# Kernel tuning notes

Measured on AMD Instinct MI355X. Metric: run time of the kernel, lower is better.

## Reference

```python
import jax, jax.numpy as jnp
import numpy as np

N_LAYERS = 6
D_MODEL = 512
D_FFN = 2048
N_STATE = 64
KSIZE = 31
BATCH = 8
SEQ = 2048
IN_SIZE = 80


def _ln(x, g, b, eps=1e-5):
    m = jnp.mean(x, axis=-1, keepdims=True)
    v = jnp.mean((x - m) ** 2, axis=-1, keepdims=True)
    return (x - m) * jax.lax.rsqrt(v + eps) * g + b


def _ffn(x, g, b, w1, b1, w2, b2):
    # LayerNorm -> Linear(D->F) -> GELU -> Linear(F->D)  (PositionalwiseFeedForward)
    h = jax.nn.gelu(_ln(x, g, b) @ w1 + b1)
    return h @ w2 + b2


def _dss(x, lam_re, lam_im, c_re, c_im, d_skip, log_dt, w_out, b_out):
    # Diagonal state-space (DSS-EXP): generate length-T kernel from diagonal poles,
    # apply causal conv via FFT, skip D*u, GELU, GLU output projection.
    Bx, T, H = x.shape
    dt = jnp.exp(log_dt)
    lam = -jnp.exp(lam_re) + 1j * lam_im                        # [N] stable poles (Re<0)
    P = jnp.exp(lam[:, None] * (dt * jnp.arange(T))[None, :])   # [N, T]
    C = c_re + 1j * c_im                                        # [H, N]
    kern = jnp.einsum('hn,nt->ht', C, P).real * dt              # [H, T]
    u = x.transpose(0, 2, 1)                                    # [B, H, T]
    n = 2 * T
    y = jnp.fft.irfft(jnp.fft.rfft(u, n=n) * jnp.fft.rfft(kern, n=n), n=n)[..., :T]
    y = y + d_skip[None, :, None] * u
    y = jax.nn.gelu(y.transpose(0, 2, 1))                       # [B, T, H]
    z = y @ w_out + b_out                                       # [B, T, 2H]
    a, g = jnp.split(z, 2, axis=-1)
    return a * jax.nn.sigmoid(g)                                # GLU


def _conv_module(x, g1, b1, bw, bb, dw, db, g2, b2, lw, lb):
    # LN -> 1x1 conv to 2D + GLU -> depthwise conv (SAME, k=31) -> LN -> GELU -> Linear
    y = _ln(x, g1, b1)
    y = y @ bw.T + bb                                           # [B, T, 2D]
    a, g = jnp.split(y, 2, axis=-1)
    y = a * jax.nn.sigmoid(g)                                   # GLU over channels
    yc = y.transpose(0, 2, 1)                                   # [B, D, T]
    yc = jax.lax.conv_general_dilated(
        yc, dw[:, None, :], (1,), 'SAME',
        feature_group_count=yc.shape[1],
        dimension_numbers=('NCH', 'OIH', 'NCH'))
    yc = yc + db[None, :, None]
    y = jax.nn.gelu(_ln(yc.transpose(0, 2, 1), g2, b2))
    return y @ lw.T + lb


def _forward(src, speaker_embs, src_w, src_b,
             ffn1_ln_g, ffn1_ln_b, ffn1_w1, ffn1_b1, ffn1_w2, ffn1_b2,
             norm1_g, norm1_b,
             lam_re, lam_im, c_re, c_im, ssm_d, log_dt, dss_out_w, dss_out_b,
             conv_ln_g, conv_ln_b, bneck_w, bneck_b, dw_w, dw_b,
             conv_ln2_g, conv_ln2_b, conv_lin_w, conv_lin_b,
             ffn2_ln_g, ffn2_ln_b, ffn2_w1, ffn2_b1, ffn2_w2, ffn2_b2,
             norm2_g, norm2_b, final_g, final_b):
    x = src @ src_w + src_b                                     # custom_src_module Linear
    for i in range(N_LAYERS):
        x = x + 0.5 * _ffn(x, ffn1_ln_g[i], ffn1_ln_b[i], ffn1_w1[i], ffn1_b1[i], ffn1_w2[i], ffn1_b2[i])
        skip = x
        x = _ln(x, norm1_g[i], norm1_b[i])
        x = _dss(x, lam_re[i], lam_im[i], c_re[i], c_im[i], ssm_d[i], log_dt[i], dss_out_w[i], dss_out_b[i])
        x = x + skip
        x = x + _conv_module(x, conv_ln_g[i], conv_ln_b[i], bneck_w[i], bneck_b[i], dw_w[i], dw_b[i],
                             conv_ln2_g[i], conv_ln2_b[i], conv_lin_w[i], conv_lin_b[i])
        x = _ln(x + 0.5 * _ffn(x, ffn2_ln_g[i], ffn2_ln_b[i], ffn2_w1[i], ffn2_b1[i], ffn2_w2[i], ffn2_b2[i]),
                norm2_g[i], norm2_b[i])
    x = _ln(x, final_g, final_b, eps=1e-6)
    return x + speaker_embs


def setup_inputs() -> dict:
    key = jax.random.key(0)
    ks = iter(jax.random.split(key, 64))
    def rn(shape, s=0.02):
        return (jax.random.normal(next(ks), shape) * s).astype(jnp.float32)
    L, D, F, N, K = N_LAYERS, D_MODEL, D_FFN, N_STATE, KSIZE
    return dict(
        src=jax.random.normal(next(ks), (BATCH, SEQ, IN_SIZE), dtype=jnp.float32),
        speaker_embs=jax.random.normal(next(ks), (BATCH, 1, D), dtype=jnp.float32),
        src_w=rn((IN_SIZE, D)), src_b=jnp.zeros((D,), jnp.float32),
        ffn1_ln_g=jnp.ones((L, D), jnp.float32), ffn1_ln_b=jnp.zeros((L, D), jnp.float32),
        ffn1_w1=rn((L, D, F)), ffn1_b1=jnp.zeros((L, F), jnp.float32),
        ffn1_w2=rn((L, F, D)), ffn1_b2=jnp.zeros((L, D), jnp.float32),
        norm1_g=jnp.ones((L, D), jnp.float32), norm1_b=jnp.zeros((L, D), jnp.float32),
        lam_re=rn((L, N), 0.5), lam_im=rn((L, N), 3.0),
        c_re=rn((L, D, N), 0.1), c_im=rn((L, D, N), 0.1),
        ssm_d=rn((L, D), 1.0), log_dt=jnp.full((L,), float(np.log(0.01)), jnp.float32),
        dss_out_w=rn((L, D, 2 * D)), dss_out_b=jnp.zeros((L, 2 * D), jnp.float32),
        conv_ln_g=jnp.ones((L, D), jnp.float32), conv_ln_b=jnp.zeros((L, D), jnp.float32),
        bneck_w=rn((L, 2 * D, D)), bneck_b=jnp.zeros((L, 2 * D), jnp.float32),
        dw_w=rn((L, D, K), 0.1), dw_b=jnp.zeros((L, D), jnp.float32),
        conv_ln2_g=jnp.ones((L, D), jnp.float32), conv_ln2_b=jnp.zeros((L, D), jnp.float32),
        conv_lin_w=rn((L, D, D)), conv_lin_b=jnp.zeros((L, D), jnp.float32),
        ffn2_ln_g=jnp.ones((L, D), jnp.float32), ffn2_ln_b=jnp.zeros((L, D), jnp.float32),
        ffn2_w1=rn((L, D, F)), ffn2_b1=jnp.zeros((L, F), jnp.float32),
        ffn2_w2=rn((L, F, D)), ffn2_b2=jnp.zeros((L, D), jnp.float32),
        norm2_g=jnp.ones((L, D), jnp.float32), norm2_b=jnp.zeros((L, D), jnp.float32),
        final_g=jnp.ones((D,), jnp.float32), final_b=jnp.zeros((D,), jnp.float32),
    )


def reference(src, speaker_embs, src_w, src_b,
              ffn1_ln_g, ffn1_ln_b, ffn1_w1, ffn1_b1, ffn1_w2, ffn1_b2,
              norm1_g, norm1_b,
              lam_re, lam_im, c_re, c_im, ssm_d, log_dt, dss_out_w, dss_out_b,
              conv_ln_g, conv_ln_b, bneck_w, bneck_b, dw_w, dw_b,
              conv_ln2_g, conv_ln2_b, conv_lin_w, conv_lin_b,
              ffn2_ln_g, ffn2_ln_b, ffn2_w1, ffn2_b1, ffn2_w2, ffn2_b2,
              norm2_g, norm2_b, final_g, final_b):
    return _forward(src, speaker_embs, src_w, src_b,
                    ffn1_ln_g, ffn1_ln_b, ffn1_w1, ffn1_b1, ffn1_w2, ffn1_b2,
                    norm1_g, norm1_b,
                    lam_re, lam_im, c_re, c_im, ssm_d, log_dt, dss_out_w, dss_out_b,
                    conv_ln_g, conv_ln_b, bneck_w, bneck_b, dw_w, dw_b,
                    conv_ln2_g, conv_ln2_b, conv_lin_w, conv_lin_b,
                    ffn2_ln_g, ffn2_ln_b, ffn2_w1, ffn2_b1, ffn2_w2, ffn2_b2,
                    norm2_g, norm2_b, final_g, final_b)
```

## Files before the change

kernel.cpp:

```cpp
#include <hip/hip_runtime.h>
#include <hip/hip_bf16.h>
#include <stdint.h>


#define NL 6
#define TT 2048
#define BB 8
#define DD 512
#define FF 2048
#define ROWS (BB*TT)

typedef __attribute__((ext_vector_type(4))) float f32x4;
typedef __attribute__((ext_vector_type(8))) short s16x8;

#define DEVI __device__ __forceinline__

DEVI float bf2f(uint32_t u) { union { uint32_t i; float f; } v; v.i = u << 16; return v.f; }
DEVI uint16_t f2bf(float f) {
    union { float f; uint32_t i; } v; v.f = f;
    uint32_t x = v.i;
    return (uint16_t)((x + 0x7fffu + ((x >> 16) & 1u)) >> 16);
}
DEVI float gelu_f(float x) {
    float x2 = x * x;
    float z  = x * fmaf(x2, 0.07135481627f, 1.5957691216f);
    return x * __builtin_amdgcn_rcpf(1.0f + __expf(-z));
}
DEVI float sigm(float x) { return __builtin_amdgcn_rcpf(1.0f + __expf(-x)); }

DEVI void gload16(const uint16_t* g, uint16_t* l) {
    __builtin_amdgcn_global_load_lds((const __attribute__((address_space(1))) void*)g,
                                     (__attribute__((address_space(3))) void*)l, 16, 0, 0);
}

__global__ void k_wtrans(const float* __restrict__ src, uint16_t* __restrict__ dst,
                         int K, int N) {
    __shared__ float tile[32][33];
    int l = blockIdx.z;
    const float* s = src + (size_t)l * K * N;
    uint16_t*    d = dst + (size_t)l * N * K;
    int n0 = blockIdx.x * 32, k0 = blockIdx.y * 32;
    int tx = threadIdx.x, ty = threadIdx.y;
#pragma unroll
    for (int i = 0; i < 4; i++) {
        int k = k0 + ty + i * 8;
        tile[ty + i * 8][tx] = s[(size_t)k * N + n0 + tx];
    }
    __syncthreads();
#pragma unroll
    for (int i = 0; i < 4; i++) {
        int n = n0 + ty + i * 8;
        d[(size_t)n * K + k0 + tx] = f2bf(tile[tx][ty + i * 8]);
    }
}
__global__ void k_wcvt(const float* __restrict__ src, uint16_t* __restrict__ dst, int n) {
    int i = blockIdx.x * 256 + threadIdx.x;
    if (i < n) dst[i] = f2bf(src[i]);
}
__global__ void k_dwt(const float* __restrict__ dw, float* __restrict__ dwt) {
    int i = blockIdx.x * 256 + threadIdx.x;
    int tot = NL * DD * 31;
    if (i >= tot) return;
    int l = i / (DD * 31), r = i % (DD * 31), d = r / 31, k = r % 31;
    dwt[(size_t)l * 31 * DD + k * DD + d] = dw[i];
}
__global__ void k_srcpad(const float* __restrict__ src, uint16_t* __restrict__ dst) {
    int i = blockIdx.x * 256 + threadIdx.x;
    if (i >= ROWS * 128) return;
    int r = i >> 7, c = i & 127;
    dst[i] = (c < 80) ? f2bf(src[(size_t)r * 80 + c]) : (uint16_t)0;
}
__global__ void k_wsrcpad(const float* __restrict__ w, uint16_t* __restrict__ dst) {
    int i = blockIdx.x * 256 + threadIdx.x;
    if (i >= DD * 128) return;
    int n = i >> 7, k = i & 127;
    dst[i] = (k < 80) ? f2bf(w[(size_t)k * DD + n]) : (uint16_t)0;
}

template <int MODE>
__global__ void k_ln(const float* __restrict__ in, void* __restrict__ outp,
                     const float* __restrict__ gam, const float* __restrict__ bet,
                     const float* __restrict__ spk, float eps) {
    int row  = blockIdx.x * 4 + (threadIdx.x >> 6);
    int lane = threadIdx.x & 63;
    const float* x = in + (size_t)row * DD;
    float4 a0 = *(const float4*)&x[lane * 4];
    float4 a1 = *(const float4*)&x[256 + lane * 4];
    float v[8] = {a0.x, a0.y, a0.z, a0.w, a1.x, a1.y, a1.z, a1.w};
    float s = 0.f, q = 0.f;
#pragma unroll
    for (int i = 0; i < 8; i++) { s += v[i]; q += v[i] * v[i]; }
#pragma unroll
    for (int m = 1; m < 64; m <<= 1) { s += __shfl_xor(s, m); q += __shfl_xor(q, m); }
    float mean = s * (1.0f / 512.0f);
    float var  = fmaxf(q * (1.0f / 512.0f) - mean * mean, 0.0f);
    float inv  = rsqrtf(var + eps);
    float4 g0 = *(const float4*)&gam[lane * 4];
    float4 g1 = *(const float4*)&gam[256 + lane * 4];
    float4 b0 = *(const float4*)&bet[lane * 4];
    float4 b1 = *(const float4*)&bet[256 + lane * 4];
    float gv[8] = {g0.x, g0.y, g0.z, g0.w, g1.x, g1.y, g1.z, g1.w};
    float bv[8] = {b0.x, b0.y, b0.z, b0.w, b1.x, b1.y, b1.z, b1.w};
    float y[8];
#pragma unroll
    for (int i = 0; i < 8; i++) y[i] = (v[i] - mean) * inv * gv[i] + bv[i];
    uint16_t* o = (uint16_t*)outp + (size_t)row * DD;
    uint2 p0, p1;
    p0.x = (uint32_t)f2bf(y[0]) | ((uint32_t)f2bf(y[1]) << 16);
    p0.y = (uint32_t)f2bf(y[2]) | ((uint32_t)f2bf(y[3]) << 16);
    p1.x = (uint32_t)f2bf(y[4]) | ((uint32_t)f2bf(y[5]) << 16);
    p1.y = (uint32_t)f2bf(y[6]) | ((uint32_t)f2bf(y[7]) << 16);
    *(uint2*)&o[lane * 4]       = p0;
    *(uint2*)&o[256 + lane * 4] = p1;
}

template <int M2>
__global__ void k_ln2(const float* __restrict__ in, float* __restrict__ X,
                      void* __restrict__ out2,
                      const float* __restrict__ g1, const float* __restrict__ b1,
                      const float* __restrict__ g2, const float* __restrict__ b2,
                      const float* __restrict__ spk, float eps2) {
    int row  = blockIdx.x * 4 + (threadIdx.x >> 6);
    int lane = threadIdx.x & 63;
    const float* x = in + (size_t)row * DD;
    float4 a0 = *(const float4*)&x[lane * 4];
    float4 a1 = *(const float4*)&x[256 + lane * 4];
    float v[8] = {a0.x, a0.y, a0.z, a0.w, a1.x, a1.y, a1.z, a1.w};
    float s = 0.f, q = 0.f;
#pragma unroll
    for (int i = 0; i < 8; i++) { s += v[i]; q += v[i] * v[i]; }
#pragma unroll
    for (int m = 1; m < 64; m <<= 1) { s += __shfl_xor(s, m); q += __shfl_xor(q, m); }
    float mean = s * (1.0f / 512.0f);
    float var  = fmaxf(q * (1.0f / 512.0f) - mean * mean, 0.0f);
    float inv  = rsqrtf(var + 1e-5f);
    float4 g0 = *(const float4*)&g1[lane * 4];
    float4 g1v = *(const float4*)&g1[256 + lane * 4];
    float4 b0 = *(const float4*)&b1[lane * 4];
    float4 b1v = *(const float4*)&b1[256 + lane * 4];
    float gv[8] = {g0.x, g0.y, g0.z, g0.w, g1v.x, g1v.y, g1v.z, g1v.w};
    float bv[8] = {b0.x, b0.y, b0.z, b0.w, b1v.x, b1v.y, b1v.z, b1v.w};
    float y[8];
    float s2 = 0.f, q2 = 0.f;
#pragma unroll
    for (int i = 0; i < 8; i++) {
        y[i] = (v[i] - mean) * inv * gv[i] + bv[i];
        s2 += y[i]; q2 += y[i] * y[i];
    }
    if (M2 == 6) {
        float* xo = X + (size_t)row * DD;
        *(float4*)&xo[lane * 4]       = make_float4(y[0], y[1], y[2], y[3]);
        *(float4*)&xo[256 + lane * 4] = make_float4(y[4], y[5], y[6], y[7]);
    }
#pragma unroll
    for (int m = 1; m < 64; m <<= 1) { s2 += __shfl_xor(s2, m); q2 += __shfl_xor(q2, m); }
    float mean2 = s2 * (1.0f / 512.0f);
    float var2  = fmaxf(q2 * (1.0f / 512.0f) - mean2 * mean2, 0.0f);
    float inv2  = rsqrtf(var2 + eps2);
    float4 G0 = *(const float4*)&g2[lane * 4];
    float4 G1 = *(const float4*)&g2[256 + lane * 4];
    float4 B0 = *(const float4*)&b2[lane * 4];
    float4 B1v = *(const float4*)&b2[256 + lane * 4];
    float Gv[8] = {G0.x, G0.y, G0.z, G0.w, G1.x, G1.y, G1.z, G1.w};
    float Bv[8] = {B0.x, B0.y, B0.z, B0.w, B1v.x, B1v.y, B1v.z, B1v.w};
    float z[8];
#pragma unroll
    for (int i = 0; i < 8; i++) z[i] = (y[i] - mean2) * inv2 * Gv[i] + Bv[i];
    if (M2 == 6) {
        uint16_t* o = (uint16_t*)out2 + (size_t)row * DD;
        uint2 p0, p1;
        p0.x = (uint32_t)f2bf(z[0]) | ((uint32_t)f2bf(z[1]) << 16);
        p0.y = (uint32_t)f2bf(z[2]) | ((uint32_t)f2bf(z[3]) << 16);
        p1.x = (uint32_t)f2bf(z[4]) | ((uint32_t)f2bf(z[5]) << 16);
        p1.y = (uint32_t)f2bf(z[6]) | ((uint32_t)f2bf(z[7]) << 16);
        *(uint2*)&o[lane * 4]       = p0;
        *(uint2*)&o[256 + lane * 4] = p1;
    } else {
        const float* sp = spk + (size_t)(row >> 11) * DD;
        float4 s0 = *(const float4*)&sp[lane * 4];
        float4 s1 = *(const float4*)&sp[256 + lane * 4];
        float* o = (float*)out2 + (size_t)row * DD;
        *(float4*)&o[lane * 4]       = make_float4(z[0]+s0.x, z[1]+s0.y, z[2]+s0.z, z[3]+s0.w);
        *(float4*)&o[256 + lane * 4] = make_float4(z[4]+s1.x, z[5]+s1.y, z[6]+s1.z, z[7]+s1.w);
    }
}

__global__ void k_gluln(const uint16_t* __restrict__ H, float* __restrict__ X,
                        uint16_t* __restrict__ out,
                        const float* __restrict__ gam, const float* __restrict__ bet) {
    int row  = blockIdx.x * 4 + (threadIdx.x >> 6);
    int lane = threadIdx.x & 63;
    const uint16_t* hr = H + (size_t)row * 1024;
    uint2 ha0 = *(const uint2*)&hr[lane * 4];
    uint2 ha1 = *(const uint2*)&hr[256 + lane * 4];
    uint2 hg0 = *(const uint2*)&hr[512 + lane * 4];
    uint2 hg1 = *(const uint2*)&hr[768 + lane * 4];
    uint32_t aw[4] = {ha0.x, ha0.y, ha1.x, ha1.y};
    uint32_t gw[4] = {hg0.x, hg0.y, hg1.x, hg1.y};
    float* xr = X + (size_t)row * DD;
    float4 x0 = *(const float4*)&xr[lane * 4];
    float4 x1 = *(const float4*)&xr[256 + lane * 4];
    float xv[8] = {x0.x, x0.y, x0.z, x0.w, x1.x, x1.y, x1.z, x1.w};
    float v[8];
#pragma unroll
    for (int p = 0; p < 4; p++) {
        float a0 = bf2f(aw[p] & 0xffffu), a1 = bf2f(aw[p] >> 16);
        float g0 = bf2f(gw[p] & 0xffffu), g1 = bf2f(gw[p] >> 16);
        v[2*p]   = xv[2*p]   + a0 * sigm(g0);
        v[2*p+1] = xv[2*p+1] + a1 * sigm(g1);
    }
    *(float4*)&xr[lane * 4]       = make_float4(v[0], v[1], v[2], v[3]);
    *(float4*)&xr[256 + lane * 4] = make_float4(v[4], v[5], v[6], v[7]);
    float s = 0.f, q = 0.f;
#pragma unroll
    for (int i = 0; i < 8; i++) { s += v[i]; q += v[i] * v[i]; }
#pragma unroll
    for (int m = 1; m < 64; m <<= 1) { s += __shfl_xor(s, m); q += __shfl_xor(q, m); }
    float mean = s * (1.0f / 512.0f);
    float var  = fmaxf(q * (1.0f / 512.0f) - mean * mean, 0.0f);
    float inv  = rsqrtf(var + 1e-5f);
    float4 g0 = *(const float4*)&gam[lane * 4];
    float4 g1 = *(const float4*)&gam[256 + lane * 4];
    float4 b0 = *(const float4*)&bet[lane * 4];
    float4 b1 = *(const float4*)&bet[256 + lane * 4];
    float gv[8] = {g0.x, g0.y, g0.z, g0.w, g1.x, g1.y, g1.z, g1.w};
    float bv[8] = {b0.x, b0.y, b0.z, b0.w, b1.x, b1.y, b1.z, b1.w};
    uint16_t* o = out + (size_t)row * DD;
    uint2 p0, p1;
    float y0 = (v[0]-mean)*inv*gv[0]+bv[0], y1 = (v[1]-mean)*inv*gv[1]+bv[1];
    float y2 = (v[2]-mean)*inv*gv[2]+bv[2], y3 = (v[3]-mean)*inv*gv[3]+bv[3];
    float y4 = (v[4]-mean)*inv*gv[4]+bv[4], y5 = (v[5]-mean)*inv*gv[5]+bv[5];
    float y6 = (v[6]-mean)*inv*gv[6]+bv[6], y7 = (v[7]-mean)*inv*gv[7]+bv[7];
    p0.x = (uint32_t)f2bf(y0) | ((uint32_t)f2bf(y1) << 16);
    p0.y = (uint32_t)f2bf(y2) | ((uint32_t)f2bf(y3) << 16);
    p1.x = (uint32_t)f2bf(y4) | ((uint32_t)f2bf(y5) << 16);
    p1.y = (uint32_t)f2bf(y6) | ((uint32_t)f2bf(y7) << 16);
    *(uint2*)&o[lane * 4]       = p0;
    *(uint2*)&o[256 + lane * 4] = p1;
}

template <int MODE, int BN>
__global__ __launch_bounds__(512, 2) void k_gemm3(
    const uint16_t* __restrict__ A, const uint16_t* __restrict__ Bt,
    const float* __restrict__ bias, int M, int N, int K,
    void* __restrict__ outp, float* __restrict__ X) {
    constexpr int MR = 8;
    constexpr int NR = BN / 64;
    constexpr int ABLK = 16;
    constexpr int BBLK = BN / 16;
    constexpr int APW = 2;
    constexpr int BPW = BBLK / 8;
    constexpr int LV  = APW + BPW;
    __shared__ __align__(16) uint16_t As[3][ABLK * 512];
    __shared__ __align__(16) uint16_t Bs[3][BBLK * 512];
    int tid = threadIdx.x;
    int wave = tid >> 6, lane = tid & 63;
    int l15 = lane & 15, l16 = lane >> 4;
    int wr = wave >> 2, wc = wave & 3;

    int nwg = gridDim.x;
    int q8  = nwg >> 3;
    int wg  = (blockIdx.x & 7) * q8 + (blockIdx.x >> 3);
    int nbx = M >> 8;
    int bx = wg % nbx, by = wg / nbx;
    int m0 = bx * 256, n0 = by * BN;

    const uint16_t* srcA[APW];
    const uint16_t* srcB[BPW];
#pragma unroll
    for (int p = 0; p < APW; p++) {
        int bi = wave * APW + p;
        srcA[p] = A + (size_t)(m0 + bi * 16 + l15) * K + l16 * 8;
    }
#pragma unroll
    for (int p = 0; p < BPW; p++) {
        int bi = wave * BPW + p;
        srcB[p] = Bt + (size_t)(n0 + bi * 16 + l15) * K + l16 * 8;
    }

    f32x4 acc[MR][NR];
#pragma unroll
    for (int i = 0; i < MR; i++)
#pragma unroll
        for (int j = 0; j < NR; j++) acc[i][j] = (f32x4){0.f, 0.f, 0.f, 0.f};

    auto STAGE = [&](int tt) {
        int b = tt % 3;
        int kof = tt << 5;
#pragma unroll
        for (int p = 0; p < APW; p++)
            gload16(srcA[p] + kof, &As[b][(wave * APW + p) * 512]);
#pragma unroll
        for (int p = 0; p < BPW; p++)
            gload16(srcB[p] + kof, &Bs[b][(wave * BPW + p) * 512]);
    };

    int nk = K >> 5;
    STAGE(0);
    STAGE(1);
    for (int t = 0; t < nk; ++t) {
        if (t + 1 < nk) {
            if (LV == 4) asm volatile("s_waitcnt vmcnt(4)" ::: "memory");
            else         asm volatile("s_waitcnt vmcnt(3)" ::: "memory");
        } else {
            asm volatile("s_waitcnt vmcnt(0)" ::: "memory");
        }
        __builtin_amdgcn_s_barrier();
        asm volatile("" ::: "memory");
        if (t + 2 < nk) STAGE(t + 2);
        int buf = t % 3;
        s16x8 af[MR], bfr[NR];
#pragma unroll
        for (int i = 0; i < MR; i++)
            af[i] = *(const s16x8*)&As[buf][(wr * MR + i) * 512 + lane * 8];
#pragma unroll
        for (int j = 0; j < NR; j++)
            bfr[j] = *(const s16x8*)&Bs[buf][(wc * NR + j) * 512 + lane * 8];
#pragma unroll
        for (int i = 0; i < MR; i++)
#pragma unroll
            for (int j = 0; j < NR; j++)
                acc[i][j] = __builtin_amdgcn_mfma_f32_16x16x32_bf16(af[i], bfr[j], acc[i][j], 0, 0, 0);
    }
#pragma unroll
    for (int i = 0; i < MR; i++) {
#pragma unroll
        for (int j = 0; j < NR; j++) {
            int gcol = n0 + wc * NR * 16 + j * 16 + l15;
            float bv = bias[gcol];
#pragma unroll
            for (int q = 0; q < 4; q++) {
                int grow = m0 + wr * MR * 16 + i * 16 + l16 * 4 + q;
                float v = acc[i][j][q] + bv;
                if (MODE == 0) {
                    ((uint16_t*)outp)[(size_t)grow * N + gcol] = f2bf(gelu_f(v));
                } else if (MODE == 1) {
                    ((uint16_t*)outp)[(size_t)grow * N + gcol] = f2bf(v);
                } else if (MODE == 2) {
                    X[(size_t)grow * DD + gcol] += 0.5f * v;
                } else if (MODE == 3) {
                    X[(size_t)grow * DD + gcol] += v;
                } else if (MODE == 4) {
                    ((float*)outp)[(size_t)grow * DD + gcol] =
                        X[(size_t)grow * DD + gcol] + 0.5f * v;
                } else {
                    X[(size_t)grow * DD + gcol] = v;
                }
            }
        }
    }
}

__global__ void k_tpose(const uint16_t* __restrict__ in, uint16_t* __restrict__ out,
                        int R, int C) {
    __shared__ uint16_t tile[32][33];
    size_t boff = (size_t)blockIdx.z * R * C;
    int c0 = blockIdx.x * 32, r0 = blockIdx.y * 32;
    int tx = threadIdx.x, ty = threadIdx.y;
#pragma unroll
    for (int i = 0; i < 4; i++)
        tile[ty + i * 8][tx] = in[boff + (size_t)(r0 + ty + i * 8) * C + c0 + tx];
    __syncthreads();
#pragma unroll
    for (int i = 0; i < 4; i++)
        out[boff + (size_t)(c0 + ty + i * 8) * R + r0 + tx] = tile[tx][ty + i * 8];
}

__global__ __launch_bounds__(64) void k_phiprep(
        const float* __restrict__ lam_re, const float* __restrict__ lam_im,
        const float* __restrict__ log_dt, uint16_t* __restrict__ PHI,
        float* __restrict__ A64f) {
    int l = blockIdx.x, n = threadIdx.x;
    float dt = expf(log_dt[l]);
    float lr = lam_re[l * 64 + n], li = lam_im[l * 64 + n];
    float mag = expf(-expf(lr) * dt), th = li * dt;
    float Are = mag * __cosf(th), Aim = mag * __sinf(th);
    float Pre = 1.f, Pim = 0.f;
    uint16_t* ph = PHI + (size_t)l * 8192;
    for (int tau = 0; tau < 64; tau++) {
        int s = 63 - tau;
        ph[n * 64 + s]        = f2bf(Pre);
        ph[(64 + n) * 64 + s] = f2bf(Pim);
        float nr = Pre * Are - Pim * Aim;
        float ni = Pre * Aim + Pim * Are;
        Pre = nr; Pim = ni;
    }
    A64f[l * 128 + 2 * n]     = Pre;
    A64f[l * 128 + 2 * n + 1] = Pim;
}

__global__ __launch_bounds__(64) void k_gprep(
        const float* __restrict__ lam_re, const float* __restrict__ lam_im,
        const float* __restrict__ c_re, const float* __restrict__ c_im,
        const float* __restrict__ ssm_d, const float* __restrict__ log_dt,
        int l, uint16_t* __restrict__ G) {
    int h = blockIdx.x, n = threadIdx.x;
    __shared__ float klds[64];
    float dt = expf(log_dt[l]);
    float lr = lam_re[l * 64 + n], li = lam_im[l * 64 + n];
    float mag = expf(-expf(lr) * dt), th = li * dt;
    float Are = mag * __cosf(th), Aim = mag * __sinf(th);
    float Cre = c_re[(size_t)l * DD * 64 + h * 64 + n];
    float Cim = c_im[(size_t)l * DD * 64 + h * 64 + n];
    uint16_t* Gh = G + (size_t)h * 64 * 192;
    float Pre = 1.f, Pim = 0.f;
    for (int r = 0; r < 64; r++) {
        float t = Cre * Pre - Cim * Pim;
        float s = t;
        s += __shfl_xor(s, 1);  s += __shfl_xor(s, 2);  s += __shfl_xor(s, 4);
        s += __shfl_xor(s, 8);  s += __shfl_xor(s, 16); s += __shfl_xor(s, 32);
        if (n == 0) klds[r] = dt * s;
        float nr = Pre * Are - Pim * Aim;
        float ni = Pre * Aim + Pim * Are;
        float wre = dt * (Cre * nr - Cim * ni);
        float wim = dt * (Cre * ni + Cim * nr);
        Gh[r * 192 + 64 + n]  = f2bf(wre);
        Gh[r * 192 + 128 + n] = f2bf(-wim);
        Pre = nr; Pim = ni;
    }
    __syncthreads();
    float dh = ssm_d[l * DD + h];
    for (int r = 0; r < 64; r++) {
        int c = n;
        float val = (c < r) ? klds[r - c] : (c == r ? klds[0] + dh : 0.f);
        Gh[r * 192 + c] = f2bf(val);
    }
}

__global__ __launch_bounds__(256) void k_pass1(
        const uint16_t* __restrict__ u, const uint16_t* __restrict__ PHI,
        uint16_t* __restrict__ E) {
    __shared__ __align__(16) uint16_t Phs[128 * 72];
    int tid = threadIdx.x;
    for (int v = tid; v < 1024; v += 256) {
        int row = v >> 3, kb = v & 7;
        *(s16x8*)&Phs[row * 72 + kb * 8] = *(const s16x8*)&PHI[row * 64 + kb * 8];
    }
    __syncthreads();
    int wave = tid >> 6, lane = tid & 63;
    int l15 = lane & 15, l16 = lane >> 4;
    int m0 = (wave & 1) * 64;
    int colbase = blockIdx.x * 128 + (wave >> 1) * 64;
    f32x4 acc[4][4];
#pragma unroll
    for (int i = 0; i < 4; i++)
#pragma unroll
        for (int j = 0; j < 4; j++) acc[i][j] = (f32x4){0.f, 0.f, 0.f, 0.f};
#pragma unroll
    for (int kt = 0; kt < 64; kt += 32) {
        s16x8 a[4], b[4];
#pragma unroll
        for (int i = 0; i < 4; i++)
            a[i] = *(const s16x8*)&Phs[(m0 + i * 16 + l15) * 72 + kt + l16 * 8];
#pragma unroll
        for (int j = 0; j < 4; j++)
            b[j] = *(const s16x8*)(u + (size_t)(colbase + j * 16 + l15) * 64 + kt + l16 * 8);
#pragma unroll
        for (int i = 0; i < 4; i++)
#pragma unroll
            for (int j = 0; j < 4; j++)
                acc[i][j] = __builtin_amdgcn_mfma_f32_16x16x32_bf16(a[i], b[j], acc[i][j], 0, 0, 0);
    }
#pragma unroll
    for (int i = 0; i < 4; i++)
#pragma unroll
        for (int j = 0; j < 4; j++) {
            int col = colbase + j * 16 + l15;
            int r0  = m0 + i * 16 + l16 * 4;
            uint32_t p0 = (uint32_t)f2bf(acc[i][j][0]) | ((uint32_t)f2bf(acc[i][j][1]) << 16);
            uint32_t p1 = (uint32_t)f2bf(acc[i][j][2]) | ((uint32_t)f2bf(acc[i][j][3]) << 16);
            *(uint2*)&E[(size_t)col * 128 + r0] = make_uint2(p0, p1);
        }
}

__global__ void k_pass2(const uint16_t* __restrict__ E, const float* __restrict__ A64f,
                        int l, uint16_t* __restrict__ Sp) {
    int gid = blockIdx.x * 256 + threadIdx.x;
    int n = gid & 63, bh = gid >> 6;
    int b = bh >> 9, h = bh & 511;
    float2 A = *(const float2*)&A64f[l * 128 + 2 * n];
    float Sre = 0.f, Sim = 0.f;
    const uint16_t* Eb = E + (size_t)bh * 32 * 128;
    uint16_t* So = Sp + (size_t)h * 32768 + (size_t)b * 32 * 128;
    for (int i = 0; i < 32; i++) {
        So[i * 128 + n]      = f2bf(Sre);
        So[i * 128 + 64 + n] = f2bf(Sim);
        float er = bf2f((uint32_t)Eb[i * 128 + n]);
        float ei = bf2f((uint32_t)Eb[i * 128 + 64 + n]);
        float nr = A.x * Sre - A.y * Sim + er;
        float ni = A.x * Sim + A.y * Sre + ei;
        Sre = nr; Sim = ni;
    }
}

__global__ __launch_bounds__(256) void k_pass3(
        const uint16_t* __restrict__ G, const uint16_t* __restrict__ u,
        const uint16_t* __restrict__ Sp, uint16_t* __restrict__ Y) {
    __shared__ __align__(16) uint16_t Gs[64 * 200];
    int h = blockIdx.x, tid = threadIdx.x;
    for (int v = tid; v < 1536; v += 256) {
        int row = v / 24, kb = v % 24;
        *(s16x8*)&Gs[row * 200 + kb * 8] = *(const s16x8*)&G[(size_t)h * 12288 + row * 192 + kb * 8];
    }
    __syncthreads();
    int wave = tid >> 6, lane = tid & 63;
    int l15 = lane & 15, l16 = lane >> 4;
    int wn = wave * 64;
    const uint16_t* uh = u + (size_t)h * TT;
    const uint16_t* sh = Sp + (size_t)h * 32768;
    f32x4 acc[4][4];
#pragma unroll
    for (int i = 0; i < 4; i++)
#pragma unroll
        for (int j = 0; j < 4; j++) acc[i][j] = (f32x4){0.f, 0.f, 0.f, 0.f};
#pragma unroll
    for (int kt = 0; kt < 192; kt += 32) {
        s16x8 a[4], b[4];
#pragma unroll
        for (int i = 0; i < 4; i++)
            a[i] = *(const s16x8*)&Gs[(i * 16 + l15) * 200 + kt + l16 * 8];
#pragma unroll
        for (int j = 0; j < 4; j++) {
            int col = wn + j * 16 + l15;
            const uint16_t* src;
            if (kt < 64)
                src = uh + (size_t)(col >> 5) * (DD * TT) + (col & 31) * 64 + kt + l16 * 8;
            else
                src = sh + (size_t)col * 128 + (kt - 64) + l16 * 8;
            b[j] = *(const s16x8*)src;
        }
#pragma unroll
        for (int i = 0; i < 4; i++)
#pragma unroll
            for (int j = 0; j < 4; j++)
                acc[i][j] = __builtin_amdgcn_mfma_f32_16x16x32_bf16(a[i], b[j], acc[i][j], 0, 0, 0);
    }
#pragma unroll
    for (int i = 0; i < 4; i++)
#pragma unroll
        for (int j = 0; j < 4; j++) {
            int col = wn + j * 16 + l15;
            int r0  = i * 16 + l16 * 4;
            uint16_t* dst = Y + (size_t)(col >> 5) * (DD * TT) + (size_t)h * TT + (col & 31) * 64 + r0;
            uint32_t p0 = (uint32_t)f2bf(acc[i][j][0]) | ((uint32_t)f2bf(acc[i][j][1]) << 16);
            uint32_t p1 = (uint32_t)f2bf(acc[i][j][2]) | ((uint32_t)f2bf(acc[i][j][3]) << 16);
            *(uint2*)&dst[0] = make_uint2(p0, p1);
        }
}

__global__ void k_tgelu(const uint16_t* __restrict__ y, uint16_t* __restrict__ out) {
    __shared__ uint16_t tile[32][33];
    int b = blockIdx.z;
    int t0 = blockIdx.x * 32, h0 = blockIdx.y * 32;
    int tx = threadIdx.x, ty = threadIdx.y;
    const uint16_t* yb = y + (size_t)b * DD * TT;
#pragma unroll
    for (int i = 0; i < 4; i++) {
        int h = h0 + ty + i * 8;
        tile[ty + i * 8][tx] = f2bf(gelu_f(bf2f((uint32_t)yb[(size_t)h * TT + t0 + tx])));
    }
    __syncthreads();
    uint16_t* ob = out + (size_t)b * TT * DD;
#pragma unroll
    for (int i = 0; i < 4; i++) {
        int t = t0 + ty + i * 8;
        ob[(size_t)t * DD + h0 + tx] = tile[tx][ty + i * 8];
    }
}

__global__ void k_glu(const uint16_t* __restrict__ z, uint16_t* __restrict__ out) {
    int i = blockIdx.x * 256 + threadIdx.x;
    int r = i >> 8;
    int c = (i & 255) * 2;
    uint32_t av = *(const uint32_t*)&z[(size_t)r * 1024 + c];
    uint32_t gv = *(const uint32_t*)&z[(size_t)r * 1024 + 512 + c];
    float a0 = bf2f(av & 0xffffu), a1 = bf2f(av >> 16);
    float g0 = bf2f(gv & 0xffffu), g1 = bf2f(gv >> 16);
    float v0 = a0 * sigm(g0), v1 = a1 * sigm(g1);
    uint32_t p = (uint32_t)f2bf(v0) | ((uint32_t)f2bf(v1) << 16);
    *(uint32_t*)&out[(size_t)r * DD + c] = p;
}

__global__ __launch_bounds__(256) void k_dwln(
        const uint16_t* __restrict__ in, const float* __restrict__ dwt,
        const float* __restrict__ db, const float* __restrict__ gam,
        const float* __restrict__ bet, uint16_t* __restrict__ out) {
    __shared__ __align__(16) uint16_t xs[34 * 512];
    __shared__ float red[4][4][2];
    int tid = threadIdx.x;
    int t0 = (blockIdx.x & 511) * 4;
    int b  = blockIdx.x >> 9;
    const uint16_t* ib = in + (size_t)b * TT * DD;
    for (int v = tid; v < 34 * 64; v += 256) {
        int row = v >> 6, seg = v & 63;
        int tj = t0 - 15 + row;
        uint4 val = make_uint4(0, 0, 0, 0);
        if (tj >= 0 && tj < TT) val = *(const uint4*)&ib[(size_t)tj * DD + seg * 8];
        *(uint4*)&xs[row * 512 + seg * 8] = val;
    }
    __syncthreads();
    int d = tid * 2;
    int wave = tid >> 6, lane = tid & 63;
    float a0[4], a1[4];
    float bv0 = db[d], bv1 = db[d + 1];
#pragma unroll
    for (int o = 0; o < 4; o++) { a0[o] = bv0; a1[o] = bv1; }
#pragma unroll
    for (int k = 0; k < 31; k++) {
        float2 w = *(const float2*)&dwt[k * DD + d];
#pragma unroll
        for (int o = 0; o < 4; o++) {
            uint32_t v = *(const uint32_t*)&xs[(o + k) * 512 + d];
            a0[o] = fmaf(bf2f(v & 0xffffu), w.x, a0[o]);
            a1[o] = fmaf(bf2f(v >> 16), w.y, a1[o]);
        }
    }
#pragma unroll
    for (int o = 0; o < 4; o++) {
        float ss = a0[o] + a1[o];
        float qq = a0[o] * a0[o] + a1[o] * a1[o];
#pragma unroll
        for (int m = 1; m < 64; m <<= 1) { ss += __shfl_xor(ss, m); qq += __shfl_xor(qq, m); }
        if (lane == 0) { red[o][wave][0] = ss; red[o][wave][1] = qq; }
    }
    __syncthreads();
    float g0 = gam[d], g1 = gam[d + 1], be0 = bet[d], be1 = bet[d + 1];
#pragma unroll
    for (int o = 0; o < 4; o++) {
        float s = red[o][0][0] + red[o][1][0] + red[o][2][0] + red[o][3][0];
        float q = red[o][0][1] + red[o][1][1] + red[o][2][1] + red[o][3][1];
        float mean = s * (1.0f / 512.0f);
        float var  = fmaxf(q * (1.0f / 512.0f) - mean * mean, 0.0f);
        float inv  = rsqrtf(var + 1e-5f);
        float y0 = gelu_f((a0[o] - mean) * inv * g0 + be0);
        float y1 = gelu_f((a1[o] - mean) * inv * g1 + be1);
        uint32_t p = (uint32_t)f2bf(y0) | ((uint32_t)f2bf(y1) << 16);
        *(uint32_t*)&out[((size_t)b * TT + t0 + o) * DD + d] = p;
    }
}

extern "C" void kernel_launch(void* const* d_in, const int* in_sizes, int n_in,
                              void* d_out, int out_size, void* d_ws, size_t ws_size,
                              hipStream_t stream) {
    const float* src        = (const float*)d_in[0];
    const float* speaker    = (const float*)d_in[1];
    const float* src_w      = (const float*)d_in[2];
    const float* src_b      = (const float*)d_in[3];
    const float* ffn1_ln_g  = (const float*)d_in[4];
    const float* ffn1_ln_b  = (const float*)d_in[5];
    const float* ffn1_w1    = (const float*)d_in[6];
    const float* ffn1_b1    = (const float*)d_in[7];
    const float* ffn1_w2    = (const float*)d_in[8];
    const float* ffn1_b2    = (const float*)d_in[9];
    const float* norm1_g    = (const float*)d_in[10];
    const float* norm1_b    = (const float*)d_in[11];
    const float* lam_re     = (const float*)d_in[12];
    const float* lam_im     = (const float*)d_in[13];
    const float* c_re       = (const float*)d_in[14];
    const float* c_im       = (const float*)d_in[15];
    const float* ssm_d      = (const float*)d_in[16];
    const float* log_dt     = (const float*)d_in[17];
    const float* dss_out_w  = (const float*)d_in[18];
    const float* dss_out_b  = (const float*)d_in[19];
    const float* conv_ln_g  = (const float*)d_in[20];
    const float* conv_ln_b  = (const float*)d_in[21];
    const float* bneck_w    = (const float*)d_in[22];
    const float* bneck_b    = (const float*)d_in[23];
    const float* dw_w       = (const float*)d_in[24];
    const float* dw_b       = (const float*)d_in[25];
    const float* conv_ln2_g = (const float*)d_in[26];
    const float* conv_ln2_b = (const float*)d_in[27];
    const float* conv_lin_w = (const float*)d_in[28];
    const float* conv_lin_b = (const float*)d_in[29];
    const float* ffn2_ln_g  = (const float*)d_in[30];
    const float* ffn2_ln_b  = (const float*)d_in[31];
    const float* ffn2_w1    = (const float*)d_in[32];
    const float* ffn2_b1    = (const float*)d_in[33];
    const float* ffn2_w2    = (const float*)d_in[34];
    const float* ffn2_b2    = (const float*)d_in[35];
    const float* norm2_g    = (const float*)d_in[36];
    const float* norm2_b    = (const float*)d_in[37];
    const float* final_g    = (const float*)d_in[38];
    const float* final_b    = (const float*)d_in[39];
    (void)in_sizes; (void)n_in; (void)out_size; (void)ws_size;

    uint8_t* ws = (uint8_t*)d_ws;
    float*    X   = (float*)   (ws + 0);
    float*    F0  = (float*)   (ws + 33554432);
    uint16_t* B1  = (uint16_t*)(ws + 67108864);
    uint16_t* B2  = (uint16_t*)(ws + 83886080);
    uint16_t* B3  = (uint16_t*)(ws + 100663296);
    uint16_t* H   = (uint16_t*)(ws + 117440512);
    uint16_t* Wf1a= (uint16_t*)(ws + 184549376);
    uint16_t* Wf1b= (uint16_t*)(ws + 197132288);
    uint16_t* Wds = (uint16_t*)(ws + 209715200);
    uint16_t* Wbn = (uint16_t*)(ws + 216006656);
    uint16_t* Wcl = (uint16_t*)(ws + 222298112);
    uint16_t* Wf2a= (uint16_t*)(ws + 225443840);
    uint16_t* Wf2b= (uint16_t*)(ws + 238026752);
    float*    DWT = (float*)   (ws + 250609664);
    uint16_t* PHI = (uint16_t*)(ws + 250990592);
    float*    A64f= (float*)   (ws + 251088896);

    uint16_t* GBUF = B1;
    uint16_t* SPK  = (uint16_t*)F0;
    uint16_t* EBUF = H;
    uint16_t* SRCB = B3;
    uint16_t* WSRC = B2;

    dim3 tb(32, 8);
    k_wtrans<<<dim3(FF/32, DD/32, NL), tb, 0, stream>>>(ffn1_w1, Wf1a, DD, FF);
    k_wtrans<<<dim3(DD/32, FF/32, NL), tb, 0, stream>>>(ffn1_w2, Wf1b, FF, DD);
    k_wtrans<<<dim3(1024/32, DD/32, NL), tb, 0, stream>>>(dss_out_w, Wds, DD, 1024);
    k_wcvt<<<(NL*1024*DD + 255)/256, 256, 0, stream>>>(bneck_w, Wbn, NL*1024*DD);
    k_wcvt<<<(NL*DD*DD + 255)/256, 256, 0, stream>>>(conv_lin_w, Wcl, NL*DD*DD);
    k_wtrans<<<dim3(FF/32, DD/32, NL), tb, 0, stream>>>(ffn2_w1, Wf2a, DD, FF);
    k_wtrans<<<dim3(DD/32, FF/32, NL), tb, 0, stream>>>(ffn2_w2, Wf2b, FF, DD);
    k_dwt<<<(NL*DD*31 + 255)/256, 256, 0, stream>>>(dw_w, DWT);
    k_phiprep<<<NL, 64, 0, stream>>>(lam_re, lam_im, log_dt, PHI, A64f);
    k_srcpad<<<(ROWS*128 + 255)/256, 256, 0, stream>>>(src, SRCB);
    k_wsrcpad<<<(DD*128 + 255)/256, 256, 0, stream>>>(src_w, WSRC);

    k_gemm3<5,128><<<256, 512, 0, stream>>>(SRCB, WSRC, src_b, ROWS, DD, 128, nullptr, X);
    k_ln<0><<<4096, 256, 0, stream>>>(X, B1, ffn1_ln_g, ffn1_ln_b, nullptr, 1e-5f);

    for (int l = 0; l < NL; l++) {
        k_gemm3<0,256><<<512, 512, 0, stream>>>(B1, Wf1a + (size_t)l*FF*DD, ffn1_b1 + l*FF,
                                                ROWS, FF, DD, H, nullptr);
        k_gemm3<2,128><<<256, 512, 0, stream>>>(H, Wf1b + (size_t)l*DD*FF, ffn1_b2 + l*DD,
                                                ROWS, DD, FF, nullptr, X);
        k_ln<0><<<4096, 256, 0, stream>>>(X, B1, norm1_g + l*DD, norm1_b + l*DD, nullptr, 1e-5f);
        k_tpose<<<dim3(DD/32, TT/32, BB), tb, 0, stream>>>(B1, B2, TT, DD);
        k_gprep<<<DD, 64, 0, stream>>>(lam_re, lam_im, c_re, c_im, ssm_d, log_dt, l, GBUF);
        k_pass1<<<1024, 256, 0, stream>>>(B2, PHI + (size_t)l*8192, EBUF);
        k_pass2<<<1024, 256, 0, stream>>>(EBUF, A64f, l, SPK);
        k_pass3<<<DD, 256, 0, stream>>>(GBUF, B2, SPK, B3);
        k_tgelu<<<dim3(TT/32, DD/32, BB), tb, 0, stream>>>(B3, B1);
        k_gemm3<1,256><<<256, 512, 0, stream>>>(B1, Wds + (size_t)l*1024*DD, dss_out_b + l*1024,
                                                ROWS, 1024, DD, H, nullptr);
        k_gluln<<<4096, 256, 0, stream>>>(H, X, B1, conv_ln_g + l*DD, conv_ln_b + l*DD);
        k_gemm3<1,256><<<256, 512, 0, stream>>>(B1, Wbn + (size_t)l*1024*DD, bneck_b + l*1024,
                                                ROWS, 1024, DD, H, nullptr);
        k_glu<<<ROWS, 256, 0, stream>>>(H, B2);
        k_dwln<<<BB*512, 256, 0, stream>>>(B2, DWT + (size_t)l*31*DD, dw_b + l*DD,
                                           conv_ln2_g + l*DD, conv_ln2_b + l*DD, B1);
        k_gemm3<3,128><<<256, 512, 0, stream>>>(B1, Wcl + (size_t)l*DD*DD, conv_lin_b + l*DD,
                                                ROWS, DD, DD, nullptr, X);
        k_ln<0><<<4096, 256, 0, stream>>>(X, B1, ffn2_ln_g + l*DD, ffn2_ln_b + l*DD, nullptr, 1e-5f);
        k_gemm3<0,256><<<512, 512, 0, stream>>>(B1, Wf2a + (size_t)l*FF*DD, ffn2_b1 + l*FF,
                                                ROWS, FF, DD, H, nullptr);
        k_gemm3<4,128><<<256, 512, 0, stream>>>(H, Wf2b + (size_t)l*DD*FF, ffn2_b2 + l*DD,
                                                ROWS, DD, FF, F0, X);
        if (l < NL - 1) {
            k_ln2<6><<<4096, 256, 0, stream>>>(F0, X, B1, norm2_g + l*DD, norm2_b + l*DD,
                                               ffn1_ln_g + (l+1)*DD, ffn1_ln_b + (l+1)*DD,
                                               nullptr, 1e-5f);
        } else {
            k_ln2<7><<<4096, 256, 0, stream>>>(F0, nullptr, d_out, norm2_g + l*DD, norm2_b + l*DD,
                                               final_g, final_b, speaker, 1e-6f);
        }
    }
}
```

Measured before the change: 3.657 ms.

## Rework GEMM to 4-wave double-buffered tiles and fuse bottleneck GLU epilogue

The GEMM kernel moves from 8 waves per block with a 3-stage vmcnt-tuned pipeline to 4 waves per block, each computing a larger per-wave tile, with simple double buffering synchronised by __syncthreads. The block-to-tile swizzle is also changed. The bottleneck weights and bias are row-interleaved at setup so the GLU can be computed in the GEMM epilogue via a lane shuffle, which removes the separate k_glu kernel and its round trip of the 1024-wide intermediate. Transpose tile padding changes from 33 to 34. Per-wave register pressure and the weaker latency hiding of the new pipeline may offset the gains.

```diff
diff --git a/kernel.cpp b/kernel.cpp
--- a/kernel.cpp
+++ b/kernel.cpp
@@ -56,6 +56,21 @@
 __global__ void k_wcvt(const float* __restrict__ src, uint16_t* __restrict__ dst, int n) {
     int i = blockIdx.x * 256 + threadIdx.x;
     if (i < n) dst[i] = f2bf(src[i]);
+}
+__global__ void k_wglu(const float* __restrict__ w, const float* __restrict__ b,
+                       uint16_t* __restrict__ wd, float* __restrict__ bd) {
+    int i = blockIdx.x * 256 + threadIdx.x;
+    int tot = NL * 1024 * DD;
+    if (i < tot) {
+        int l = i / (1024 * DD), r = (i / DD) % 1024, k = i % DD;
+        int srow = (r & 1) ? (512 + (r >> 1)) : (r >> 1);
+        wd[i] = f2bf(w[((size_t)l * 1024 + srow) * DD + k]);
+    }
+    if (i < NL * 1024) {
+        int l = i >> 10, r = i & 1023;
+        int srow = (r & 1) ? (512 + (r >> 1)) : (r >> 1);
+        bd[i] = b[l * 1024 + srow];
+    }
 }
 __global__ void k_dwt(const float* __restrict__ dw, float* __restrict__ dwt) {
     int i = blockIdx.x * 256 + threadIdx.x;
@@ -240,29 +255,28 @@
 }
 
 template <int MODE, int BN>
-__global__ __launch_bounds__(512, 2) void k_gemm3(
+__global__ __launch_bounds__(256, 1) void k_gemm4(
     const uint16_t* __restrict__ A, const uint16_t* __restrict__ Bt,
     const float* __restrict__ bias, int M, int N, int K,
     void* __restrict__ outp, float* __restrict__ X) {
     constexpr int MR = 8;
-    constexpr int NR = BN / 64;
+    constexpr int NR = BN / 32;
     constexpr int ABLK = 16;
     constexpr int BBLK = BN / 16;
-    constexpr int APW = 2;
-    constexpr int BPW = BBLK / 8;
-    constexpr int LV  = APW + BPW;
-    __shared__ __align__(16) uint16_t As[3][ABLK * 512];
-    __shared__ __align__(16) uint16_t Bs[3][BBLK * 512];
+    constexpr int APW = 4;
+    constexpr int BPW = BBLK / 4;
+    __shared__ __align__(16) uint16_t As[2][ABLK * 512];
+    __shared__ __align__(16) uint16_t Bs[2][BBLK * 512];
     int tid = threadIdx.x;
     int wave = tid >> 6, lane = tid & 63;
     int l15 = lane & 15, l16 = lane >> 4;
-    int wr = wave >> 2, wc = wave & 3;
-
-    int nwg = gridDim.x;
-    int q8  = nwg >> 3;
-    int wg  = (blockIdx.x & 7) * q8 + (blockIdx.x >> 3);
-    int nbx = M >> 8;
-    int bx = wg % nbx, by = wg / nbx;
+    int wr = wave >> 1, wc = wave & 1;
+
+    int nbx  = M >> 8;
+    int nbxq = nbx >> 3;
+    int x8 = blockIdx.x & 7, jj = blockIdx.x >> 3;
+    int bx = x8 * nbxq + (jj % nbxq);
+    int by = jj / nbxq;
     int m0 = bx * 256, n0 = by * BN;
 
     const uint16_t* srcA[APW];
@@ -285,7 +299,7 @@
         for (int j = 0; j < NR; j++) acc[i][j] = (f32x4){0.f, 0.f, 0.f, 0.f};
 
     auto STAGE = [&](int tt) {
-        int b = tt % 3;
+        int b = tt & 1;
         int kof = tt << 5;
 #pragma unroll
         for (int p = 0; p < APW; p++)
@@ -297,18 +311,10 @@
 
     int nk = K >> 5;
     STAGE(0);
-    STAGE(1);
+    __syncthreads();
     for (int t = 0; t < nk; ++t) {
-        if (t + 1 < nk) {
-            if (LV == 4) asm volatile("s_waitcnt vmcnt(4)" ::: "memory");
-            else         asm volatile("s_waitcnt vmcnt(3)" ::: "memory");
-        } else {
-            asm volatile("s_waitcnt vmcnt(0)" ::: "memory");
-        }
-        __builtin_amdgcn_s_barrier();
-        asm volatile("" ::: "memory");
-        if (t + 2 < nk) STAGE(t + 2);
-        int buf = t % 3;
+        int buf = t & 1;
+        if (t + 1 < nk) STAGE(t + 1);
         s16x8 af[MR], bfr[NR];
 #pragma unroll
         for (int i = 0; i < MR; i++)
@@ -321,6 +327,7 @@
 #pragma unroll
             for (int j = 0; j < NR; j++)
                 acc[i][j] = __builtin_amdgcn_mfma_f32_16x16x32_bf16(af[i], bfr[j], acc[i][j], 0, 0, 0);
+        __syncthreads();
     }
 #pragma unroll
     for (int i = 0; i < MR; i++) {
@@ -343,8 +350,14 @@
                 } else if (MODE == 4) {
                     ((float*)outp)[(size_t)grow * DD + gcol] =
                         X[(size_t)grow * DD + gcol] + 0.5f * v;
+                } else if (MODE == 5) {
+                    X[(size_t)grow * DD + gcol] = v;
                 } else {
-                    X[(size_t)grow * DD + gcol] = v;
+                    float g = __shfl_xor(v, 1);
+                    if ((l15 & 1) == 0) {
+                        ((uint16_t*)outp)[(size_t)grow * DD + (gcol >> 1)] =
+                            f2bf(v * sigm(g));
+                    }
                 }
             }
         }
@@ -353,7 +366,7 @@
 
 __global__ void k_tpose(const uint16_t* __restrict__ in, uint16_t* __restrict__ out,
                         int R, int C) {
-    __shared__ uint16_t tile[32][33];
+    __shared__ uint16_t tile[32][34];
     size_t boff = (size_t)blockIdx.z * R * C;
     int c0 = blockIdx.x * 32, r0 = blockIdx.y * 32;
     int tx = threadIdx.x, ty = threadIdx.y;
@@ -549,7 +562,7 @@
 }
 
 __global__ void k_tgelu(const uint16_t* __restrict__ y, uint16_t* __restrict__ out) {
-    __shared__ uint16_t tile[32][33];
+    __shared__ uint16_t tile[32][34];
     int b = blockIdx.z;
     int t0 = blockIdx.x * 32, h0 = blockIdx.y * 32;
     int tx = threadIdx.x, ty = threadIdx.y;
@@ -566,19 +579,6 @@
         int t = t0 + ty + i * 8;
         ob[(size_t)t * DD + h0 + tx] = tile[tx][ty + i * 8];
     }
-}
-
-__global__ void k_glu(const uint16_t* __restrict__ z, uint16_t* __restrict__ out) {
-    int i = blockIdx.x * 256 + threadIdx.x;
-    int r = i >> 8;
-    int c = (i & 255) * 2;
-    uint32_t av = *(const uint32_t*)&z[(size_t)r * 1024 + c];
-    uint32_t gv = *(const uint32_t*)&z[(size_t)r * 1024 + 512 + c];
-    float a0 = bf2f(av & 0xffffu), a1 = bf2f(av >> 16);
-    float g0 = bf2f(gv & 0xffffu), g1 = bf2f(gv >> 16);
-    float v0 = a0 * sigm(g0), v1 = a1 * sigm(g1);
-    uint32_t p = (uint32_t)f2bf(v0) | ((uint32_t)f2bf(v1) << 16);
-    *(uint32_t*)&out[(size_t)r * DD + c] = p;
 }
 
 __global__ __launch_bounds__(256) void k_dwln(
@@ -701,6 +701,7 @@
     float*    DWT = (float*)   (ws + 250609664);
     uint16_t* PHI = (uint16_t*)(ws + 250990592);
     float*    A64f= (float*)   (ws + 251088896);
+    float*    BNB = (float*)   (ws + 251092992);
 
     uint16_t* GBUF = B1;
     uint16_t* SPK  = (uint16_t*)F0;
@@ -712,7 +713,7 @@
     k_wtrans<<<dim3(FF/32, DD/32, NL), tb, 0, stream>>>(ffn1_w1, Wf1a, DD, FF);
     k_wtrans<<<dim3(DD/32, FF/32, NL), tb, 0, stream>>>(ffn1_w2, Wf1b, FF, DD);
     k_wtrans<<<dim3(1024/32, DD/32, NL), tb, 0, stream>>>(dss_out_w, Wds, DD, 1024);
-    k_wcvt<<<(NL*1024*DD + 255)/256, 256, 0, stream>>>(bneck_w, Wbn, NL*1024*DD);
+    k_wglu<<<(NL*1024*DD + 255)/256, 256, 0, stream>>>(bneck_w, bneck_b, Wbn, BNB);
     k_wcvt<<<(NL*DD*DD + 255)/256, 256, 0, stream>>>(conv_lin_w, Wcl, NL*DD*DD);
     k_wtrans<<<dim3(FF/32, DD/32, NL), tb, 0, stream>>>(ffn2_w1, Wf2a, DD, FF);
     k_wtrans<<<dim3(DD/32, FF/32, NL), tb, 0, stream>>>(ffn2_w2, Wf2b, FF, DD);
@@ -721,13 +722,13 @@
     k_srcpad<<<(ROWS*128 + 255)/256, 256, 0, stream>>>(src, SRCB);
     k_wsrcpad<<<(DD*128 + 255)/256, 256, 0, stream>>>(src_w, WSRC);
 
-    k_gemm3<5,128><<<256, 512, 0, stream>>>(SRCB, WSRC, src_b, ROWS, DD, 128, nullptr, X);
+    k_gemm4<5,128><<<256, 256, 0, stream>>>(SRCB, WSRC, src_b, ROWS, DD, 128, nullptr, X);
     k_ln<0><<<4096, 256, 0, stream>>>(X, B1, ffn1_ln_g, ffn1_ln_b, nullptr, 1e-5f);
 
     for (int l = 0; l < NL; l++) {
-        k_gemm3<0,256><<<512, 512, 0, stream>>>(B1, Wf1a + (size_t)l*FF*DD, ffn1_b1 + l*FF,
+        k_gemm4<0,256><<<512, 256, 0, stream>>>(B1, Wf1a + (size_t)l*FF*DD, ffn1_b1 + l*FF,
                                                 ROWS, FF, DD, H, nullptr);
-        k_gemm3<2,128><<<256, 512, 0, stream>>>(H, Wf1b + (size_t)l*DD*FF, ffn1_b2 + l*DD,
+        k_gemm4<2,128><<<256, 256, 0, stream>>>(H, Wf1b + (size_t)l*DD*FF, ffn1_b2 + l*DD,
                                                 ROWS, DD, FF, nullptr, X);
         k_ln<0><<<4096, 256, 0, stream>>>(X, B1, norm1_g + l*DD, norm1_b + l*DD, nullptr, 1e-5f);
         k_tpose<<<dim3(DD/32, TT/32, BB), tb, 0, stream>>>(B1, B2, TT, DD);
@@ -736,20 +737,19 @@
         k_pass2<<<1024, 256, 0, stream>>>(EBUF, A64f, l, SPK);
         k_pass3<<<DD, 256, 0, stream>>>(GBUF, B2, SPK, B3);
         k_tgelu<<<dim3(TT/32, DD/32, BB), tb, 0, stream>>>(B3, B1);
-        k_gemm3<1,256><<<256, 512, 0, stream>>>(B1, Wds + (size_t)l*1024*DD, dss_out_b + l*1024,
+        k_gemm4<1,256><<<256, 256, 0, stream>>>(B1, Wds + (size_t)l*1024*DD, dss_out_b + l*1024,
                                                 ROWS, 1024, DD, H, nullptr);
         k_gluln<<<4096, 256, 0, stream>>>(H, X, B1, conv_ln_g + l*DD, conv_ln_b + l*DD);
-        k_gemm3<1,256><<<256, 512, 0, stream>>>(B1, Wbn + (size_t)l*1024*DD, bneck_b + l*1024,
-                                                ROWS, 1024, DD, H, nullptr);
-        k_glu<<<ROWS, 256, 0, stream>>>(H, B2);
+        k_gemm4<6,256><<<256, 256, 0, stream>>>(B1, Wbn + (size_t)l*1024*DD, BNB + l*1024,
+                                                ROWS, 1024, DD, B2, nullptr);
         k_dwln<<<BB*512, 256, 0, stream>>>(B2, DWT + (size_t)l*31*DD, dw_b + l*DD,
                                            conv_ln2_g + l*DD, conv_ln2_b + l*DD, B1);
-        k_gemm3<3,128><<<256, 512, 0, stream>>>(B1, Wcl + (size_t)l*DD*DD, conv_lin_b + l*DD,
+        k_gemm4<3,128><<<256, 256, 0, stream>>>(B1, Wcl + (size_t)l*DD*DD, conv_lin_b + l*DD,
                                                 ROWS, DD, DD, nullptr, X);
         k_ln<0><<<4096, 256, 0, stream>>>(X, B1, ffn2_ln_g + l*DD, ffn2_ln_b + l*DD, nullptr, 1e-5f);
-        k_gemm3<0,256><<<512, 512, 0, stream>>>(B1, Wf2a + (size_t)l*FF*DD, ffn2_b1 + l*FF,
+        k_gemm4<0,256><<<512, 256, 0, stream>>>(B1, Wf2a + (size_t)l*FF*DD, ffn2_b1 + l*FF,
                                                 ROWS, FF, DD, H, nullptr);
-        k_gemm3<4,128><<<256, 512, 0, stream>>>(H, Wf2b + (size_t)l*DD*FF, ffn2_b2 + l*DD,
+        k_gemm4<4,128><<<256, 256, 0, stream>>>(H, Wf2b + (size_t)l*DD*FF, ffn2_b2 + l*DD,
                                                 ROWS, DD, FF, F0, X);
         if (l < NL - 1) {
             k_ln2<6><<<4096, 256, 0, stream>>>(F0, X, B1, norm2_g + l*DD, norm2_b + l*DD,
```

New measurement: 4.167 ms. 1.14x slower.
